# Kernel optimization log

Measured on AMD Instinct MI355X. Metric: run time of the kernel, lower is better.

## Reference

```python
import jax, jax.numpy as jnp
import numpy as np

N = 100000
E = 1600000
IN_C = 256
HID = 128
OUT_C = 128
HEADS = 4
C_HEAD = HID // HEADS
BN_EPS = 1e-5
NEG_SLOPE = 0.2


def setup_inputs() -> dict:
    key = jax.random.key(0)
    ks = jax.random.split(key, 12)
    s = lambda fan: 1.0 / np.sqrt(fan)
    return {
        "x": jax.random.normal(ks[0], (N, IN_C), dtype=jnp.float32),
        "W_gat": jax.random.normal(ks[1], (IN_C, HID), dtype=jnp.float32) * s(IN_C),
        "att_src": jax.random.normal(ks[2], (HEADS, C_HEAD), dtype=jnp.float32) * s(C_HEAD),
        "att_dst": jax.random.normal(ks[3], (HEADS, C_HEAD), dtype=jnp.float32) * s(C_HEAD),
        "bias_gat": jnp.zeros((HID,), dtype=jnp.float32),
        "bn1_gamma": jnp.ones((HID,), dtype=jnp.float32),
        "bn1_beta": jnp.zeros((HID,), dtype=jnp.float32),
        "eps_gin": jnp.zeros((), dtype=jnp.float32),
        "lin_W": jax.random.normal(ks[4], (HID, OUT_C), dtype=jnp.float32) * s(HID),
        "lin_b": jnp.zeros((OUT_C,), dtype=jnp.float32),
        "bn2_gamma": jnp.ones((OUT_C,), dtype=jnp.float32),
        "bn2_beta": jnp.zeros((OUT_C,), dtype=jnp.float32),
        "edge_index": jax.random.randint(ks[5], (2, E), 0, N, dtype=jnp.int64),
    }


def batch_norm(h, gamma, beta):
    mu = jnp.mean(h, axis=0)
    var = jnp.var(h, axis=0)
    return (h - mu) * jax.lax.rsqrt(var + BN_EPS) * gamma + beta


def reference(x, W_gat, att_src, att_dst, bias_gat, bn1_gamma, bn1_beta,
              eps_gin, lin_W, lin_b, bn2_gamma, bn2_beta, edge_index):
    src, dst = edge_index[0], edge_index[1]
    # ---- GATConv ----
    h = (x @ W_gat).reshape(N, HEADS, C_HEAD)              # [N,H,C]
    a_src = jnp.einsum('nhc,hc->nh', h, att_src)            # [N,H]
    a_dst = jnp.einsum('nhc,hc->nh', h, att_dst)            # [N,H]
    e = jax.nn.leaky_relu(a_src[src] + a_dst[dst], NEG_SLOPE)  # [E,H]
    # segment softmax over incoming edges of each dst node
    m = jax.ops.segment_max(e, dst, num_segments=N)         # [N,H]
    num = jnp.exp(e - m[dst])                                # [E,H]
    den = jax.ops.segment_sum(num, dst, num_segments=N)      # [N,H]
    alpha = num / den[dst]                                   # [E,H]
    msg = alpha[:, :, None] * h[src]                         # [E,H,C]
    out1 = jax.ops.segment_sum(msg, dst, num_segments=N)     # [N,H,C]
    out1 = out1.reshape(N, HID) + bias_gat
    # BN + ELU (dropout = identity in eval)
    out1 = jax.nn.elu(batch_norm(out1, bn1_gamma, bn1_beta))
    # ---- GINConv: nn((1+eps)*x + sum_neighbors) ----
    agg = jax.ops.segment_sum(out1[src], dst, num_segments=N)
    z = (1.0 + eps_gin) * out1 + agg
    out2 = z @ lin_W + lin_b
    out2 = jax.nn.elu(batch_norm(out2, bn2_gamma, bn2_beta))
    return out2
```

## Files before the change

### kernel.cpp

```cpp
#include <hip/hip_runtime.h>

#define N_NODES 100000
#define N_EDGES 1600000
#define IN_C 256
#define HID 128
#define NEG_SLOPE 0.2f
#define BN_EPS 1e-5f
#define NBUCK 391
#define NPART 391

typedef unsigned int uint32;
typedef __attribute__((ext_vector_type(8))) short bf16x8;
typedef __attribute__((ext_vector_type(4))) float f32x4;

__device__ __forceinline__ float lrelu(float x) { return x > 0.f ? x : NEG_SLOPE * x; }

__device__ __forceinline__ unsigned short f2bf(float f) {
    uint32 u = __float_as_uint(f);
    u += 0x7fffu + ((u >> 16) & 1u);
    return (unsigned short)(u >> 16);
}
__device__ __forceinline__ float bf2f(unsigned short h) {
    return __uint_as_float(((uint32)h) << 16);
}
__device__ __forceinline__ float bflo(uint32 v) { return __uint_as_float(v << 16); }
__device__ __forceinline__ float bfhi(uint32 v) { return __uint_as_float(v & 0xffff0000u); }
__device__ __forceinline__ uint32 packbf(float a, float b) {
    return (uint32)f2bf(a) | ((uint32)f2bf(b) << 16);
}

__global__ void k_init(int* __restrict__ bcount, float* __restrict__ bnacc) {
    int t = threadIdx.x;
    if (t < NBUCK) bcount[t] = 0;
    if (t < 512) bnacc[t] = 0.f;
}

__global__ void k_transpose_all(const float* __restrict__ W1, const float* __restrict__ W2,
                                unsigned short* __restrict__ Wt1,
                                unsigned short* __restrict__ Wt2) {
    int idx = blockIdx.x * 256 + threadIdx.x;
    if (idx < IN_C * 128) {
        int k = idx >> 7, n = idx & 127;
        Wt1[n * IN_C + k] = f2bf(W1[idx]);
    } else {
        idx -= IN_C * 128;
        if (idx < HID * 128) {
            int k = idx >> 7, n = idx & 127;
            Wt2[n * HID + k] = f2bf(W2[idx]);
        }
    }
}

template <bool AF32, bool OUTF32>
__global__ __launch_bounds__(256) void k_gemm(const void* __restrict__ Av,
                                              const unsigned short* __restrict__ Wt,
                                              void* __restrict__ Out, int K) {
    __shared__ unsigned short As[128 * 72];
    __shared__ unsigned short Bs[128 * 72];
    const int t = threadIdx.x;
    const int n0 = blockIdx.x * 128;
    const int wv = t >> 6, lane = t & 63;
    const int wy = wv >> 1, wx = wv & 1;
    const int lm = lane & 15, lg = lane >> 4;
    const float* Af = (const float*)Av;
    const unsigned short* Ah = (const unsigned short*)Av;

    f32x4 acc[4][4];
#pragma unroll
    for (int i = 0; i < 4; ++i)
#pragma unroll
        for (int j = 0; j < 4; ++j) acc[i][j] = (f32x4){0.f, 0.f, 0.f, 0.f};

    float4 afp[8];
    uint4 ahp[4];
    uint4 bvp[4];

    if (AF32) {
#pragma unroll
        for (int p = 0; p < 8; ++p) {
            int idx = p * 256 + t, row = idx >> 4, c4 = idx & 15, gn = n0 + row;
            afp[p] = (gn < N_NODES) ? *(const float4*)&Af[(size_t)gn * K + c4 * 4]
                                    : make_float4(0.f, 0.f, 0.f, 0.f);
        }
    } else {
#pragma unroll
        for (int p = 0; p < 4; ++p) {
            int idx = p * 256 + t, row = idx >> 3, c = idx & 7, gn = n0 + row;
            ahp[p] = (gn < N_NODES) ? *(const uint4*)&Ah[(size_t)gn * K + c * 8]
                                    : make_uint4(0, 0, 0, 0);
        }
    }
#pragma unroll
    for (int p = 0; p < 4; ++p) {
        int idx = p * 256 + t, n = idx >> 3, c = idx & 7;
        bvp[p] = *(const uint4*)&Wt[(size_t)n * K + c * 8];
    }

    for (int kc = 0; kc < K; kc += 64) {
        if (AF32) {
#pragma unroll
            for (int p = 0; p < 8; ++p) {
                int idx = p * 256 + t, row = idx >> 4, c4 = idx & 15;
                ushort4 b;
                b.x = f2bf(afp[p].x); b.y = f2bf(afp[p].y);
                b.z = f2bf(afp[p].z); b.w = f2bf(afp[p].w);
                *(ushort4*)&As[row * 72 + c4 * 4] = b;
            }
        } else {
#pragma unroll
            for (int p = 0; p < 4; ++p) {
                int idx = p * 256 + t, row = idx >> 3, c = idx & 7;
                *(uint4*)&As[row * 72 + c * 8] = ahp[p];
            }
        }
#pragma unroll
        for (int p = 0; p < 4; ++p) {
            int idx = p * 256 + t, n = idx >> 3, c = idx & 7;
            *(uint4*)&Bs[n * 72 + c * 8] = bvp[p];
        }
        __syncthreads();
        int kn = kc + 64;
        if (kn < K) {
            if (AF32) {
#pragma unroll
                for (int p = 0; p < 8; ++p) {
                    int idx = p * 256 + t, row = idx >> 4, c4 = idx & 15, gn = n0 + row;
                    afp[p] = (gn < N_NODES) ? *(const float4*)&Af[(size_t)gn * K + kn + c4 * 4]
                                            : make_float4(0.f, 0.f, 0.f, 0.f);
                }
            } else {
#pragma unroll
                for (int p = 0; p < 4; ++p) {
                    int idx = p * 256 + t, row = idx >> 3, c = idx & 7, gn = n0 + row;
                    ahp[p] = (gn < N_NODES) ? *(const uint4*)&Ah[(size_t)gn * K + kn + c * 8]
                                            : make_uint4(0, 0, 0, 0);
                }
            }
#pragma unroll
            for (int p = 0; p < 4; ++p) {
                int idx = p * 256 + t, n = idx >> 3, c = idx & 7;
                bvp[p] = *(const uint4*)&Wt[(size_t)n * K + kn + c * 8];
            }
        }
#pragma unroll
        for (int ks = 0; ks < 2; ++ks) {
            bf16x8 af[4], bfr[4];
#pragma unroll
            for (int i = 0; i < 4; ++i)
                af[i] = *(const bf16x8*)&As[(wy * 64 + i * 16 + lm) * 72 + ks * 32 + lg * 8];
#pragma unroll
            for (int j = 0; j < 4; ++j)
                bfr[j] = *(const bf16x8*)&Bs[(wx * 64 + j * 16 + lm) * 72 + ks * 32 + lg * 8];
#pragma unroll
            for (int i = 0; i < 4; ++i)
#pragma unroll
                for (int j = 0; j < 4; ++j)
                    acc[i][j] = __builtin_amdgcn_mfma_f32_16x16x32_bf16(af[i], bfr[j],
                                                                        acc[i][j], 0, 0, 0);
        }
        __syncthreads();
    }
#pragma unroll
    for (int i = 0; i < 4; ++i) {
#pragma unroll
        for (int r = 0; r < 4; ++r) {
            int row = n0 + wy * 64 + i * 16 + lg * 4 + r;
            if (row < N_NODES) {
#pragma unroll
                for (int j = 0; j < 4; ++j) {
                    int col = wx * 64 + j * 16 + lm;
                    float v = acc[i][j][r];
                    if (OUTF32) ((float*)Out)[(size_t)row * 128 + col] = v;
                    else ((unsigned short*)Out)[(size_t)row * 128 + col] = f2bf(v);
                }
            }
        }
    }
}

__global__ __launch_bounds__(256) void k_att(const unsigned short* __restrict__ hb,
                                             const float* __restrict__ att_s,
                                             const float* __restrict__ att_d,
                                             float* __restrict__ a_src,
                                             float* __restrict__ a_dst) {
    int node = blockIdx.x * 2 + (threadIdx.x >> 7);
    int c = threadIdx.x & 127;
    float hv = bf2f(hb[(size_t)node * 128 + c]);
    float ps = hv * att_s[c];
    float pd = hv * att_d[c];
#pragma unroll
    for (int m = 1; m < 32; m <<= 1) {
        ps += __shfl_xor(ps, m);
        pd += __shfl_xor(pd, m);
    }
    if ((c & 31) == 0) {
        int head = c >> 5;
        a_src[node * 4 + head] = ps;
        a_dst[node * 4 + head] = pd;
    }
}

__global__ __launch_bounds__(256) void k_bucket_count(const int* __restrict__ ei,
                                                      int* __restrict__ bcount) {
    __shared__ int hist[NBUCK];
    for (int i = threadIdx.x; i < NBUCK; i += 256) hist[i] = 0;
    __syncthreads();
    for (int e = blockIdx.x * 256 + threadIdx.x; e < N_EDGES; e += gridDim.x * 256)
        atomicAdd(&hist[ei[N_EDGES + e] >> 8], 1);
    __syncthreads();
    for (int i = threadIdx.x; i < NBUCK; i += 256)
        if (hist[i]) atomicAdd(&bcount[i], hist[i]);
}

__global__ void k_bucket_scan(const int* __restrict__ bcount, int* __restrict__ bucket_base,
                              int* __restrict__ gcursor, int* __restrict__ row_ptr) {
    __shared__ int sh[512];
    int t = threadIdx.x;
    int v0 = (t < NBUCK) ? bcount[t] : 0;
    int val = v0;
    sh[t] = val;
    __syncthreads();
    for (int off = 1; off < 512; off <<= 1) {
        int o = (t >= off) ? sh[t - off] : 0;
        __syncthreads();
        val += o;
        sh[t] = val;
        __syncthreads();
    }
    if (t < NBUCK) {
        int e = val - v0;
        bucket_base[t] = e;
        gcursor[t] = e;
    }
    if (t == 0) {
        bucket_base[NBUCK] = N_EDGES;
        row_ptr[N_NODES] = N_EDGES;
    }
}

__global__ __launch_bounds__(256) void k_partition(const int* __restrict__ ei,
                                                   int* __restrict__ gcursor,
                                                   int* __restrict__ staging) {
    __shared__ int hist[NBUCK];
    __shared__ int base[NBUCK];
    int t = threadIdx.x;
    int e0 = blockIdx.x * 4096;
    for (int i = t; i < NBUCK; i += 256) hist[i] = 0;
    __syncthreads();
    int pk[16], cb[16];
#pragma unroll
    for (int u = 0; u < 16; ++u) {
        int e = e0 + u * 256 + t;
        cb[u] = -1;
        if (e < N_EDGES) {
            int s = ei[e], d = ei[N_EDGES + e];
            int b = d >> 8;
            int r = atomicAdd(&hist[b], 1);
            pk[u] = ((d & 255) << 17) | s;
            cb[u] = (r << 9) | b;
        }
    }
    __syncthreads();
    for (int i = t; i < NBUCK; i += 256)
        if (hist[i]) base[i] = atomicAdd(&gcursor[i], hist[i]);
    __syncthreads();
#pragma unroll
    for (int u = 0; u < 16; ++u) {
        if (cb[u] >= 0) {
            int b = cb[u] & 511, r = cb[u] >> 9;
            staging[base[b] + r] = pk[u];
        }
    }
}

__global__ __launch_bounds__(256) void k_bucket_sort(const int* __restrict__ staging,
                                                     const int* __restrict__ bucket_base,
                                                     int* __restrict__ row_ptr,
                                                     int* __restrict__ sorted_src) {
    __shared__ int hist[256];
    __shared__ int sh[256];
    int t = threadIdx.x, b = blockIdx.x;
    int lo = bucket_base[b], hi = bucket_base[b + 1];
    hist[t] = 0;
    __syncthreads();
    for (int i = lo + t; i < hi; i += 256) atomicAdd(&hist[staging[i] >> 17], 1);
    __syncthreads();
    int v0 = hist[t];
    int val = v0;
    sh[t] = val;
    __syncthreads();
    for (int off = 1; off < 256; off <<= 1) {
        int o = (t >= off) ? sh[t - off] : 0;
        __syncthreads();
        val += o;
        sh[t] = val;
        __syncthreads();
    }
    int excl = val - v0;
    int d = b * 256 + t;
    if (d < N_NODES) row_ptr[d] = lo + excl;
    hist[t] = excl;
    __syncthreads();
    for (int i = lo + t; i < hi; i += 256) {
        int p = staging[i];
        int r = atomicAdd(&hist[p >> 17], 1);
        sorted_src[lo + r] = p & 0x1FFFF;
    }
}

__global__ __launch_bounds__(256) void k_gat_agg(const uint32* __restrict__ hb32,
                                                 const float* __restrict__ a_src,
                                                 const float* __restrict__ a_dst,
                                                 const int* __restrict__ row_ptr,
                                                 const int* __restrict__ sorted_src,
                                                 uint32* __restrict__ out1b) {
    __shared__ int sbuf[4][64];
    __shared__ float wbuf[4][64][4];
    int lane = threadIdx.x & 63, wv = threadIdx.x >> 6;
    int node = blockIdx.x * 4 + wv;
    int start = row_ptr[node];
    int deg = row_ptr[node + 1] - start;
    if (deg == 0) {
        out1b[(size_t)node * 64 + lane] = 0u;
        return;
    }
    int head = lane >> 4;
    float4 ad = *(const float4*)&a_dst[node * 4];
    float4 den4 = make_float4(0.f, 0.f, 0.f, 0.f);
    float ac0[4] = {0.f, 0.f, 0.f, 0.f};
    float ac1[4] = {0.f, 0.f, 0.f, 0.f};
    for (int j0 = 0; j0 < deg; j0 += 64) {
        int j = j0 + lane;
        int s = 0;
        float4 w = make_float4(0.f, 0.f, 0.f, 0.f);
        if (j < deg) {
            s = sorted_src[start + j];
            float4 as = *(const float4*)&a_src[s * 4];
            w.x = __expf(lrelu(as.x + ad.x));
            w.y = __expf(lrelu(as.y + ad.y));
            w.z = __expf(lrelu(as.z + ad.z));
            w.w = __expf(lrelu(as.w + ad.w));
        }
        den4.x += w.x; den4.y += w.y; den4.z += w.z; den4.w += w.w;
        sbuf[wv][lane] = s;
        *(float4*)&wbuf[wv][lane][0] = w;
        __builtin_amdgcn_wave_barrier();
        int nj = min(64, deg - j0);
        int njf = nj & ~7;
        for (int jj = 0; jj < njf; jj += 8) {
#pragma unroll
            for (int u = 0; u < 8; ++u) {
                int ss = sbuf[wv][jj + u];
                float wh = wbuf[wv][jj + u][head];
                uint32 hv = hb32[((uint32)ss << 6) + lane];
                ac0[u & 3] = fmaf(wh, bflo(hv), ac0[u & 3]);
                ac1[u & 3] = fmaf(wh, bfhi(hv), ac1[u & 3]);
            }
        }
        for (int jj = njf; jj < nj; ++jj) {
            int ss = sbuf[wv][jj];
            float wh = wbuf[wv][jj][head];
            uint32 hv = hb32[((uint32)ss << 6) + lane];
            ac0[0] = fmaf(wh, bflo(hv), ac0[0]);
            ac1[0] = fmaf(wh, bfhi(hv), ac1[0]);
        }
        __builtin_amdgcn_wave_barrier();
    }
#pragma unroll
    for (int m = 1; m < 64; m <<= 1) {
        den4.x += __shfl_xor(den4.x, m);
        den4.y += __shfl_xor(den4.y, m);
        den4.z += __shfl_xor(den4.z, m);
        den4.w += __shfl_xor(den4.w, m);
    }
    float den = head == 0 ? den4.x : head == 1 ? den4.y : head == 2 ? den4.z : den4.w;
    float rden = 1.f / den;
    float acc0 = (ac0[0] + ac0[1]) + (ac0[2] + ac0[3]);
    float acc1 = (ac1[0] + ac1[1]) + (ac1[2] + ac1[3]);
    out1b[(size_t)node * 64 + lane] = packbf(acc0 * rden, acc1 * rden);
}

__global__ __launch_bounds__(256) void k_gin_agg(const uint32* __restrict__ ob32,
                                                 const int* __restrict__ row_ptr,
                                                 const int* __restrict__ sorted_src,
                                                 const float* __restrict__ eps_ptr,
                                                 uint32* __restrict__ zb32) {
    __shared__ int sbuf[4][64];
    int lane = threadIdx.x & 63, wv = threadIdx.x >> 6;
    int node = blockIdx.x * 4 + wv;
    int start = row_ptr[node];
    int deg = row_ptr[node + 1] - start;
    float ac0[4] = {0.f, 0.f, 0.f, 0.f};
    float ac1[4] = {0.f, 0.f, 0.f, 0.f};
    for (int j0 = 0; j0 < deg; j0 += 64) {
        int j = j0 + lane;
        sbuf[wv][lane] = (j < deg) ? sorted_src[start + j] : 0;
        __builtin_amdgcn_wave_barrier();
        int nj = min(64, deg - j0);
        int njf = nj & ~7;
        for (int jj = 0; jj < njf; jj += 8) {
#pragma unroll
            for (int u = 0; u < 8; ++u) {
                int ss = sbuf[wv][jj + u];
                uint32 hv = ob32[((uint32)ss << 6) + lane];
                ac0[u & 3] += bflo(hv);
                ac1[u & 3] += bfhi(hv);
            }
        }
        for (int jj = njf; jj < nj; ++jj) {
            int ss = sbuf[wv][jj];
            uint32 hv = ob32[((uint32)ss << 6) + lane];
            ac0[0] += bflo(hv);
            ac1[0] += bfhi(hv);
        }
        __builtin_amdgcn_wave_barrier();
    }
    float ep = 1.f + eps_ptr[0];
    uint32 own = ob32[((uint32)node << 6) + lane];
    float z0 = fmaf(ep, bflo(own), (ac0[0] + ac0[1]) + (ac0[2] + ac0[3]));
    float z1 = fmaf(ep, bfhi(own), (ac1[0] + ac1[1]) + (ac1[2] + ac1[3]));
    zb32[(size_t)node * 64 + lane] = packbf(z0, z1);
}

__global__ __launch_bounds__(256) void k_bnstats_bf16(const uint32* __restrict__ buf,
                                                      float* __restrict__ acc) {
    __shared__ float sh[4][64][4];
    int lane = threadIdx.x & 63, grp = threadIdx.x >> 6;
    float s0 = 0.f, s1 = 0.f, q0 = 0.f, q1 = 0.f;
    for (int r = blockIdx.x * 4 + grp; r < N_NODES; r += gridDim.x * 4) {
        uint32 v = buf[(size_t)r * 64 + lane];
        float v0 = bflo(v), v1 = bfhi(v);
        s0 += v0; s1 += v1; q0 += v0 * v0; q1 += v1 * v1;
    }
    sh[grp][lane][0] = s0; sh[grp][lane][1] = s1;
    sh[grp][lane][2] = q0; sh[grp][lane][3] = q1;
    __syncthreads();
    if (grp == 0) {
#pragma unroll
        for (int g = 1; g < 4; ++g) {
            s0 += sh[g][lane][0]; s1 += sh[g][lane][1];
            q0 += sh[g][lane][2]; q1 += sh[g][lane][3];
        }
        int c0 = lane * 2;
        atomicAdd(&acc[c0], s0);
        atomicAdd(&acc[c0 + 1], s1);
        atomicAdd(&acc[128 + c0], q0);
        atomicAdd(&acc[128 + c0 + 1], q1);
    }
}

__global__ __launch_bounds__(256) void k_bn_elu_b16(uint32* __restrict__ buf,
                                                    const float* __restrict__ acc,
                                                    const float* __restrict__ gamma,
                                                    const float* __restrict__ beta) {
    __shared__ float psc[128], psh[128];
    int t = threadIdx.x;
    if (t < 128) {
        float mu = acc[t] * (1.f / N_NODES);
        float var = acc[128 + t] * (1.f / N_NODES) - mu * mu;
        float s = rsqrtf(var + BN_EPS) * gamma[t];
        psc[t] = s;
        psh[t] = beta[t] - mu * s;
    }
    __syncthreads();
    size_t i = (size_t)blockIdx.x * 256 + t;
    if (i >= (size_t)N_NODES * 64) return;
    int c0 = (int)(i & 63) * 2;
    uint32 v = buf[i];
    float r0 = fmaf(bflo(v), psc[c0], psh[c0]);
    float r1 = fmaf(bfhi(v), psc[c0 + 1], psh[c0 + 1]);
    r0 = r0 > 0.f ? r0 : __expf(r0) - 1.f;
    r1 = r1 > 0.f ? r1 : __expf(r1) - 1.f;
    buf[i] = packbf(r0, r1);
}

__global__ __launch_bounds__(256) void k_bn_elu_out(const uint32* __restrict__ in,
                                                    const float* __restrict__ acc,
                                                    const float* __restrict__ gamma,
                                                    const float* __restrict__ beta,
                                                    float2* __restrict__ out) {
    __shared__ float psc[128], psh[128];
    int t = threadIdx.x;
    if (t < 128) {
        float mu = acc[t] * (1.f / N_NODES);
        float var = acc[128 + t] * (1.f / N_NODES) - mu * mu;
        float s = rsqrtf(var + BN_EPS) * gamma[t];
        psc[t] = s;
        psh[t] = beta[t] - mu * s;
    }
    __syncthreads();
    size_t i = (size_t)blockIdx.x * 256 + t;
    if (i >= (size_t)N_NODES * 64) return;
    int c0 = (int)(i & 63) * 2;
    uint32 v = in[i];
    float r0 = fmaf(bflo(v), psc[c0], psh[c0]);
    float r1 = fmaf(bfhi(v), psc[c0 + 1], psh[c0 + 1]);
    r0 = r0 > 0.f ? r0 : __expf(r0) - 1.f;
    r1 = r1 > 0.f ? r1 : __expf(r1) - 1.f;
    out[i] = make_float2(r0, r1);
}

extern "C" void kernel_launch(void* const* d_in, const int* in_sizes, int n_in,
                              void* d_out, int out_size, void* d_ws, size_t ws_size,
                              hipStream_t stream) {
    (void)in_sizes; (void)n_in; (void)out_size; (void)ws_size;
    const float* x       = (const float*)d_in[0];
    const float* W_gat   = (const float*)d_in[1];
    const float* att_src = (const float*)d_in[2];
    const float* att_dst = (const float*)d_in[3];
    const float* bn1_g   = (const float*)d_in[5];
    const float* bn1_b   = (const float*)d_in[6];
    const float* eps_gin = (const float*)d_in[7];
    const float* lin_W   = (const float*)d_in[8];
    const float* bn2_g   = (const float*)d_in[10];
    const float* bn2_b   = (const float*)d_in[11];
    const int*   ei      = (const int*)d_in[12];
    float* out = (float*)d_out;

    char* w = (char*)d_ws;
    size_t o = 0;
    auto take = [&](size_t b) -> char* {
        char* p = w + o;
        o += (b + 255) & ~(size_t)255;
        return p;
    };
    unsigned short* hb   = (unsigned short*)take((size_t)N_NODES * 128 * 2);
    unsigned short* Wt1  = (unsigned short*)take((size_t)128 * IN_C * 2);
    unsigned short* Wt2  = (unsigned short*)take((size_t)128 * HID * 2);
    uint32* o1b          = (uint32*)take((size_t)N_NODES * 64 * 4);
    float* a_src         = (float*)take((size_t)N_NODES * 4 * 4);
    float* a_dst         = (float*)take((size_t)N_NODES * 4 * 4);
    int*   sorted        = (int*)take((size_t)N_EDGES * 4);
    int*   staging       = (int*)take((size_t)N_EDGES * 4);
    int*   row_ptr       = (int*)take((size_t)(N_NODES + 1) * 4);
    int*   bcount        = (int*)take((NBUCK + 1) * 4);
    int*   bucket_base   = (int*)take((NBUCK + 1) * 4);
    int*   gcursor       = (int*)take((NBUCK + 1) * 4);
    float* bnacc         = (float*)take(512 * 4);
    uint32* zb  = (uint32*)hb;
    uint32* o2b = o1b;

    const int nGemmBlocks = (N_NODES + 127) / 128;
    const int nElemBlocks = (N_NODES * 64 + 255) / 256;

    k_init<<<1, 512, 0, stream>>>(bcount, bnacc);
    k_transpose_all<<<((IN_C + HID) * 128 + 255) / 256, 256, 0, stream>>>(W_gat, lin_W,
                                                                          Wt1, Wt2);
    k_gemm<true, false><<<nGemmBlocks, 256, 0, stream>>>(x, Wt1, hb, IN_C);
    k_att<<<N_NODES / 2, 256, 0, stream>>>(hb, att_src, att_dst, a_src, a_dst);
    k_bucket_count<<<256, 256, 0, stream>>>(ei, bcount);
    k_bucket_scan<<<1, 512, 0, stream>>>(bcount, bucket_base, gcursor, row_ptr);
    k_partition<<<NPART, 256, 0, stream>>>(ei, gcursor, staging);
    k_bucket_sort<<<NBUCK, 256, 0, stream>>>(staging, bucket_base, row_ptr, sorted);
    k_gat_agg<<<N_NODES / 4, 256, 0, stream>>>((const uint32*)hb, a_src, a_dst, row_ptr,
                                               sorted, o1b);
    k_bnstats_bf16<<<512, 256, 0, stream>>>(o1b, bnacc);
    k_bn_elu_b16<<<nElemBlocks, 256, 0, stream>>>(o1b, bnacc, bn1_g, bn1_b);
    k_gin_agg<<<N_NODES / 4, 256, 0, stream>>>(o1b, row_ptr, sorted, eps_gin, zb);
    k_gemm<false, false><<<nGemmBlocks, 256, 0, stream>>>(zb, Wt2, o2b, HID);
    k_bnstats_bf16<<<512, 256, 0, stream>>>(o2b, bnacc + 256);
    k_bn_elu_out<<<nElemBlocks, 256, 0, stream>>>(o2b, bnacc + 256, bn2_g, bn2_b,
                                                  (float2*)out);
}
```

Measured before the change: 548.0 us.

## Gather neighbor rows with 16-byte loads, four edges per wave in parallel

Both the GAT and GIN aggregation kernels now split each 64-lane wave into four 16-lane groups. Each group handles a different edge and loads a full 256-byte bf16 row with uint4 loads, instead of one row per wave with 4-byte loads. Partial sums are combined across the groups with xor shuffles, and only 16 lanes write the output. Padded edges are masked with zero weights. This cuts the number of load instructions and the serial edge iterations per wave, at the cost of extra cross-lane shuffles and wasted work on tail padding for low-degree nodes.

Measured after the change: 541.4 us. Within noise of the previous version (-1.2%).

```diff
diff --git a/kernel.cpp b/kernel.cpp
--- a/kernel.cpp
+++ b/kernel.cpp
@@ -308,27 +308,26 @@
     }
 }
 
-__global__ __launch_bounds__(256) void k_gat_agg(const uint32* __restrict__ hb32,
+__global__ __launch_bounds__(256) void k_gat_agg(const uint4* __restrict__ h4,
                                                  const float* __restrict__ a_src,
                                                  const float* __restrict__ a_dst,
                                                  const int* __restrict__ row_ptr,
                                                  const int* __restrict__ sorted_src,
-                                                 uint32* __restrict__ out1b) {
+                                                 uint4* __restrict__ out1b4) {
     __shared__ int sbuf[4][64];
     __shared__ float wbuf[4][64][4];
     int lane = threadIdx.x & 63, wv = threadIdx.x >> 6;
+    int sub = lane >> 4, chl = lane & 15, hd = chl >> 2;
     int node = blockIdx.x * 4 + wv;
     int start = row_ptr[node];
     int deg = row_ptr[node + 1] - start;
     if (deg == 0) {
-        out1b[(size_t)node * 64 + lane] = 0u;
+        if (lane < 16) out1b4[((uint32)node << 4) + chl] = make_uint4(0u, 0u, 0u, 0u);
         return;
     }
-    int head = lane >> 4;
     float4 ad = *(const float4*)&a_dst[node * 4];
     float4 den4 = make_float4(0.f, 0.f, 0.f, 0.f);
-    float ac0[4] = {0.f, 0.f, 0.f, 0.f};
-    float ac1[4] = {0.f, 0.f, 0.f, 0.f};
+    float acc[8] = {0.f, 0.f, 0.f, 0.f, 0.f, 0.f, 0.f, 0.f};
     for (int j0 = 0; j0 < deg; j0 += 64) {
         int j = j0 + lane;
         int s = 0;
@@ -345,27 +344,26 @@
         sbuf[wv][lane] = s;
         *(float4*)&wbuf[wv][lane][0] = w;
         __builtin_amdgcn_wave_barrier();
-        int nj = min(64, deg - j0);
-        int njf = nj & ~7;
-        for (int jj = 0; jj < njf; jj += 8) {
-#pragma unroll
-            for (int u = 0; u < 8; ++u) {
-                int ss = sbuf[wv][jj + u];
-                float wh = wbuf[wv][jj + u][head];
-                uint32 hv = hb32[((uint32)ss << 6) + lane];
-                ac0[u & 3] = fmaf(wh, bflo(hv), ac0[u & 3]);
-                ac1[u & 3] = fmaf(wh, bfhi(hv), ac1[u & 3]);
-            }
-        }
-        for (int jj = njf; jj < nj; ++jj) {
-            int ss = sbuf[wv][jj];
-            float wh = wbuf[wv][jj][head];
-            uint32 hv = hb32[((uint32)ss << 6) + lane];
-            ac0[0] = fmaf(wh, bflo(hv), ac0[0]);
-            ac1[0] = fmaf(wh, bfhi(hv), ac1[0]);
+        int nj16 = (min(64, deg - j0) + 15) & ~15;
+        for (int jj = 0; jj < nj16; jj += 16) {
+#pragma unroll
+            for (int u = 0; u < 4; ++u) {
+                int e = jj + u * 4 + sub;
+                int ss = sbuf[wv][e];
+                float wh = wbuf[wv][e][hd];
+                uint4 hv = h4[((uint32)ss << 4) + chl];
+                acc[0] += wh * bflo(hv.x); acc[1] += wh * bfhi(hv.x);
+                acc[2] += wh * bflo(hv.y); acc[3] += wh * bfhi(hv.y);
+                acc[4] += wh * bflo(hv.z); acc[5] += wh * bfhi(hv.z);
+                acc[6] += wh * bflo(hv.w); acc[7] += wh * bfhi(hv.w);
+            }
         }
         __builtin_amdgcn_wave_barrier();
     }
+#pragma unroll
+    for (int m = 16; m < 64; m <<= 1)
+#pragma unroll
+        for (int c = 0; c < 8; ++c) acc[c] += __shfl_xor(acc[c], m);
 #pragma unroll
     for (int m = 1; m < 64; m <<= 1) {
         den4.x += __shfl_xor(den4.x, m);
@@ -373,53 +371,69 @@
         den4.z += __shfl_xor(den4.z, m);
         den4.w += __shfl_xor(den4.w, m);
     }
-    float den = head == 0 ? den4.x : head == 1 ? den4.y : head == 2 ? den4.z : den4.w;
+    float den = hd == 0 ? den4.x : hd == 1 ? den4.y : hd == 2 ? den4.z : den4.w;
     float rden = 1.f / den;
-    float acc0 = (ac0[0] + ac0[1]) + (ac0[2] + ac0[3]);
-    float acc1 = (ac1[0] + ac1[1]) + (ac1[2] + ac1[3]);
-    out1b[(size_t)node * 64 + lane] = packbf(acc0 * rden, acc1 * rden);
-}
-
-__global__ __launch_bounds__(256) void k_gin_agg(const uint32* __restrict__ ob32,
+    if (lane < 16) {
+        uint4 o;
+        o.x = packbf(acc[0] * rden, acc[1] * rden);
+        o.y = packbf(acc[2] * rden, acc[3] * rden);
+        o.z = packbf(acc[4] * rden, acc[5] * rden);
+        o.w = packbf(acc[6] * rden, acc[7] * rden);
+        out1b4[((uint32)node << 4) + chl] = o;
+    }
+}
+
+__global__ __launch_bounds__(256) void k_gin_agg(const uint4* __restrict__ ob4,
                                                  const int* __restrict__ row_ptr,
                                                  const int* __restrict__ sorted_src,
                                                  const float* __restrict__ eps_ptr,
-                                                 uint32* __restrict__ zb32) {
+                                                 uint4* __restrict__ zb4) {
     __shared__ int sbuf[4][64];
+    __shared__ float mbuf[4][64];
     int lane = threadIdx.x & 63, wv = threadIdx.x >> 6;
+    int sub = lane >> 4, chl = lane & 15;
     int node = blockIdx.x * 4 + wv;
     int start = row_ptr[node];
     int deg = row_ptr[node + 1] - start;
-    float ac0[4] = {0.f, 0.f, 0.f, 0.f};
-    float ac1[4] = {0.f, 0.f, 0.f, 0.f};
+    float acc[8] = {0.f, 0.f, 0.f, 0.f, 0.f, 0.f, 0.f, 0.f};
     for (int j0 = 0; j0 < deg; j0 += 64) {
         int j = j0 + lane;
-        sbuf[wv][lane] = (j < deg) ? sorted_src[start + j] : 0;
+        int s = 0;
+        float m = 0.f;
+        if (j < deg) { s = sorted_src[start + j]; m = 1.f; }
+        sbuf[wv][lane] = s;
+        mbuf[wv][lane] = m;
         __builtin_amdgcn_wave_barrier();
-        int nj = min(64, deg - j0);
-        int njf = nj & ~7;
-        for (int jj = 0; jj < njf; jj += 8) {
-#pragma unroll
-            for (int u = 0; u < 8; ++u) {
-                int ss = sbuf[wv][jj + u];
-                uint32 hv = ob32[((uint32)ss << 6) + lane];
-                ac0[u & 3] += bflo(hv);
-                ac1[u & 3] += bfhi(hv);
-            }
-        }
-        for (int jj = njf; jj < nj; ++jj) {
-            int ss = sbuf[wv][jj];
-            uint32 hv = ob32[((uint32)ss << 6) + lane];
-            ac0[0] += bflo(hv);
-            ac1[0] += bfhi(hv);
+        int nj16 = (min(64, deg - j0) + 15) & ~15;
+        for (int jj = 0; jj < nj16; jj += 16) {
+#pragma unroll
+            for (int u = 0; u < 4; ++u) {
+                int e = jj + u * 4 + sub;
+                int ss = sbuf[wv][e];
+                float mm = mbuf[wv][e];
+                uint4 hv = ob4[((uint32)ss << 4) + chl];
+                acc[0] += mm * bflo(hv.x); acc[1] += mm * bfhi(hv.x);
+                acc[2] += mm * bflo(hv.y); acc[3] += mm * bfhi(hv.y);
+                acc[4] += mm * bflo(hv.z); acc[5] += mm * bfhi(hv.z);
+                acc[6] += mm * bflo(hv.w); acc[7] += mm * bfhi(hv.w);
+            }
         }
         __builtin_amdgcn_wave_barrier();
     }
-    float ep = 1.f + eps_ptr[0];
-    uint32 own = ob32[((uint32)node << 6) + lane];
-    float z0 = fmaf(ep, bflo(own), (ac0[0] + ac0[1]) + (ac0[2] + ac0[3]));
-    float z1 = fmaf(ep, bfhi(own), (ac1[0] + ac1[1]) + (ac1[2] + ac1[3]));
-    zb32[(size_t)node * 64 + lane] = packbf(z0, z1);
+#pragma unroll
+    for (int m = 16; m < 64; m <<= 1)
+#pragma unroll
+        for (int c = 0; c < 8; ++c) acc[c] += __shfl_xor(acc[c], m);
+    if (lane < 16) {
+        float ep = 1.f + eps_ptr[0];
+        uint4 own = ob4[((uint32)node << 4) + chl];
+        uint4 o;
+        o.x = packbf(fmaf(ep, bflo(own.x), acc[0]), fmaf(ep, bfhi(own.x), acc[1]));
+        o.y = packbf(fmaf(ep, bflo(own.y), acc[2]), fmaf(ep, bfhi(own.y), acc[3]));
+        o.z = packbf(fmaf(ep, bflo(own.z), acc[4]), fmaf(ep, bfhi(own.z), acc[5]));
+        o.w = packbf(fmaf(ep, bflo(own.w), acc[6]), fmaf(ep, bfhi(own.w), acc[7]));
+        zb4[((uint32)node << 4) + chl] = o;
+    }
 }
 
 __global__ __launch_bounds__(256) void k_bnstats_bf16(const uint32* __restrict__ buf,
@@ -552,11 +566,12 @@
     k_bucket_scan<<<1, 512, 0, stream>>>(bcount, bucket_base, gcursor, row_ptr);
     k_partition<<<NPART, 256, 0, stream>>>(ei, gcursor, staging);
     k_bucket_sort<<<NBUCK, 256, 0, stream>>>(staging, bucket_base, row_ptr, sorted);
-    k_gat_agg<<<N_NODES / 4, 256, 0, stream>>>((const uint32*)hb, a_src, a_dst, row_ptr,
-                                               sorted, o1b);
+    k_gat_agg<<<N_NODES / 4, 256, 0, stream>>>((const uint4*)hb, a_src, a_dst, row_ptr,
+                                               sorted, (uint4*)o1b);
     k_bnstats_bf16<<<512, 256, 0, stream>>>(o1b, bnacc);
     k_bn_elu_b16<<<nElemBlocks, 256, 0, stream>>>(o1b, bnacc, bn1_g, bn1_b);
-    k_gin_agg<<<N_NODES / 4, 256, 0, stream>>>(o1b, row_ptr, sorted, eps_gin, zb);
+    k_gin_agg<<<N_NODES / 4, 256, 0, stream>>>((const uint4*)o1b, row_ptr, sorted,
+                                               eps_gin, (uint4*)zb);
     k_gemm<false, false><<<nGemmBlocks, 256, 0, stream>>>(zb, Wt2, o2b, HID);
     k_bnstats_bf16<<<512, 256, 0, stream>>>(o2b, bnacc + 256);
     k_bn_elu_out<<<nElemBlocks, 256, 0, stream>>>(o2b, bnacc + 256, bn2_g, bn2_b,
```
